# Optimization experiments

Hardware: AMD Instinct MI355X
Metric: run time of the kernel (lower is better)

The kernel has to match this reference:

```python
import jax, jax.numpy as jnp
import numpy as np

INPUT, HIDDEN = 15, 20

def setup_inputs() -> dict:
    key = jax.random.key(0)
    k1, k2, k3, k4, k5 = jax.random.split(key, 5)
    B, T = 4096, 512
    s = 1.0 / np.sqrt(HIDDEN)  # torch default uniform init bound
    feature = jax.random.normal(k1, (B, T, INPUT), dtype=jnp.float32)
    W_ih = jax.random.uniform(k2, (HIDDEN, INPUT), jnp.float32, -s, s)
    W_hh = jax.random.uniform(k3, (HIDDEN, HIDDEN), jnp.float32, -s, s)
    b_ih = jax.random.uniform(k4, (HIDDEN,), jnp.float32, -s, s)
    b_hh = jax.random.uniform(k5, (HIDDEN,), jnp.float32, -s, s)
    return {"feature": feature, "W_ih": W_ih, "W_hh": W_hh, "b_ih": b_ih, "b_hh": b_hh}

def reference(feature, W_ih, W_hh, b_ih, b_hh):
    # h_t = tanh(x_t @ W_ih^T + b_ih + h_{t-1} @ W_hh^T + b_hh)
    B, T, _ = feature.shape
    # precompute input projections for all timesteps: [T, B, H]
    xp = jnp.einsum('bti,hi->tbh', feature, W_ih) + (b_ih + b_hh)
    h0 = jnp.zeros((B, HIDDEN), dtype=feature.dtype)
    def step(h, x_t):
        h_new = jnp.tanh(x_t + h @ W_hh.T)
        return h_new, None
    hn, _ = jax.lax.scan(step, h0, xp)
    return hn  # [B, H] == hn.squeeze() for num_layers=1
```

## Files before the change

kernel.cpp:

```cpp
#include <hip/hip_runtime.h>
#include <cstddef>


typedef float g4 __attribute__((ext_vector_type(4), aligned(4)));
typedef float g2 __attribute__((ext_vector_type(2), aligned(4)));
typedef _Float16 h2  __attribute__((ext_vector_type(2)));
typedef _Float16 v8h __attribute__((ext_vector_type(8)));
typedef _Float16 v4h __attribute__((ext_vector_type(4)));

#define TT 512
#define IN 15
#define HD 20
#define CH 32
#define NCH (TT / CH)
#define XROW 16
#define XGRP (CH * XROW + 16)
#define XBUF (3 * XGRP)
#define HROW 24

#define P2(v, i) __builtin_shufflevector(v, v, 2 * (i), 2 * (i) + 1)
#define FD(acc, p, w) acc = __builtin_amdgcn_fdot2(p, w, acc, false)

__global__ __launch_bounds__(64) void rnn_fused(
    const float* __restrict__ feature, const float* __restrict__ W_ih,
    const float* __restrict__ W_hh, const float* __restrict__ b_ih,
    const float* __restrict__ b_hh, float* __restrict__ out, int B) {
  __shared__ __align__(16) _Float16 xh[2 * XBUF];
  __shared__ __align__(16) _Float16 hh[4 * HROW];

  const int lane = threadIdx.x;
  const int g = lane / HD;
  const int j = lane - g * HD;
  const int gx = (g < 3) ? g : 2;
  const int bid = blockIdx.x;
  const int b = bid * 3 + g;

  if (lane < 48) ((float*)hh)[lane] = 0.f;

  h2 wih[8];
  {
    const float* wr = W_ih + j * IN;
#pragma unroll
    for (int i = 0; i < 7; ++i)
      wih[i] = (h2){(_Float16)wr[2 * i], (_Float16)wr[2 * i + 1]};
    wih[7] = (h2){(_Float16)wr[14], (_Float16)0.f};
  }
  h2 whh[10];
  {
    const float* wr = W_hh + j * HD;
#pragma unroll
    for (int i = 0; i < 10; ++i)
      whh[i] = (h2){(_Float16)wr[2 * i], (_Float16)wr[2 * i + 1]};
  }
  const float bias = b_ih[j] + b_hh[j];

  const int grA = lane >> 5;
  const int tcA = lane & 31;
  const int bc = B - 1;
  const int bA = min(bid * 3 + grA, bc);
  const int bB = min(bid * 3 + 2, bc);
  const float* baseA = feature + ((size_t)bA * TT + tcA) * IN;
  const float* baseB = feature + ((size_t)bB * TT + tcA) * IN;

  g4 rA0, rA1, rA2; g2 rA3; float rA4;
  g4 rB0, rB1, rB2; g2 rB3; float rB4;

  auto issue = [&](int t0) {
    const float* s = baseA + (size_t)t0 * IN;
    rA0 = *(const g4*)(s);      rA1 = *(const g4*)(s + 4);
    rA2 = *(const g4*)(s + 8);  rA3 = *(const g2*)(s + 12);
    rA4 = s[14];
    if (lane < 32) {
      const float* s2 = baseB + (size_t)t0 * IN;
      rB0 = *(const g4*)(s2);     rB1 = *(const g4*)(s2 + 4);
      rB2 = *(const g4*)(s2 + 8); rB3 = *(const g2*)(s2 + 12);
      rB4 = s2[14];
    }
  };
  auto commit = [&](int bsel) {
    v8h lo = {(_Float16)rA0.x, (_Float16)rA0.y, (_Float16)rA0.z, (_Float16)rA0.w,
              (_Float16)rA1.x, (_Float16)rA1.y, (_Float16)rA1.z, (_Float16)rA1.w};
    v8h hi = {(_Float16)rA2.x, (_Float16)rA2.y, (_Float16)rA2.z, (_Float16)rA2.w,
              (_Float16)rA3.x, (_Float16)rA3.y, (_Float16)rA4,   (_Float16)0.f};
    _Float16* d = xh + bsel * XBUF + grA * XGRP + tcA * XROW;
    *(v8h*)d = lo; *((v8h*)d + 1) = hi;
    if (lane < 32) {
      v8h lo2 = {(_Float16)rB0.x, (_Float16)rB0.y, (_Float16)rB0.z, (_Float16)rB0.w,
                 (_Float16)rB1.x, (_Float16)rB1.y, (_Float16)rB1.z, (_Float16)rB1.w};
      v8h hi2 = {(_Float16)rB2.x, (_Float16)rB2.y, (_Float16)rB2.z, (_Float16)rB2.w,
                 (_Float16)rB3.x, (_Float16)rB3.y, (_Float16)rB4,   (_Float16)0.f};
      _Float16* d2 = xh + bsel * XBUF + 2 * XGRP + tcA * XROW;
      *(v8h*)d2 = lo2; *((v8h*)d2 + 1) = hi2;
    }
  };

  issue(0);
  commit(0);

  float hn = 0.f;
  const _Float16* hrd = hh + g * HROW;
  _Float16* hwr = hh + g * HROW + j;
  for (int c = 0; c < NCH; ++c) {
    if (c + 1 < NCH) issue((c + 1) * CH);
    const _Float16* xg = xh + (c & 1) * XBUF + gx * XGRP;
#pragma unroll 4
    for (int tc = 0; tc < CH; ++tc) {
      v8h ha = *(const v8h*)hrd;
      v8h hb = *(const v8h*)(hrd + 8);
      v4h hc = *(const v4h*)(hrd + 16);
      const v8h* xp = (const v8h*)(xg + tc * XROW);
      v8h xa = xp[0], xb = xp[1];
      float a0 = bias, a1 = 0.f, a2 = 0.f, a3 = 0.f;
      FD(a0, P2(xa, 0), wih[0]); FD(a1, P2(xa, 1), wih[1]);
      FD(a2, P2(xa, 2), wih[2]); FD(a3, P2(xa, 3), wih[3]);
      FD(a0, P2(xb, 0), wih[4]); FD(a1, P2(xb, 1), wih[5]);
      FD(a2, P2(xb, 2), wih[6]); FD(a3, P2(xb, 3), wih[7]);
      FD(a0, P2(ha, 0), whh[0]); FD(a1, P2(ha, 1), whh[1]);
      FD(a2, P2(ha, 2), whh[2]); FD(a3, P2(ha, 3), whh[3]);
      FD(a0, P2(hb, 0), whh[4]); FD(a1, P2(hb, 1), whh[5]);
      FD(a2, P2(hb, 2), whh[6]); FD(a3, P2(hb, 3), whh[7]);
      FD(a0, P2(hc, 0), whh[8]); FD(a1, P2(hc, 1), whh[9]);
      float s = (a0 + a1) + (a2 + a3);
      float e = exp2f(s * 2.8853900817779268f);
      hn = 1.f - 2.f * __builtin_amdgcn_rcpf(1.f + e);
      *hwr = (_Float16)hn;
    }
    if (c + 1 < NCH) commit((c + 1) & 1);
  }
  if (g < 3 && b < B) out[(size_t)b * HD + j] = hn;
}

extern "C" void kernel_launch(void* const* d_in, const int* in_sizes, int n_in,
                              void* d_out, int out_size, void* d_ws, size_t ws_size,
                              hipStream_t stream) {
  const float* feature = (const float*)d_in[0];
  const float* W_ih    = (const float*)d_in[1];
  const float* W_hh    = (const float*)d_in[2];
  const float* b_ih    = (const float*)d_in[3];
  const float* b_hh    = (const float*)d_in[4];
  float* out = (float*)d_out;
  const int B = in_sizes[0] / (TT * IN);
  const int grid = (B + 2) / 3;
  rnn_fused<<<grid, 64, 0, stream>>>(feature, W_ih, W_hh, b_ih, b_hh, out, B);
}
```

Before: 232.3 us.

## Rewrite RNN recurrence with MFMA over 16-batch tiles per wavefront

Replaces the per-lane fdot2 recurrence, which ran three batches per 64-lane block, with MFMA matrix instructions. Each wavefront now handles 16 batches, and the hidden state stays in registers as the MFMA B operand, so there is no LDS round trip for h. The input projection for the next step is computed with a separate MFMA while the current step runs, and the tanh scale is folded into the weights. Input staging is reworked into 16-step double-buffered chunks. The grid shrinks to B/16 blocks, so there are far fewer waves to fill the GPU, and every step now depends on MFMA latency.

```diff
diff --git a/kernel.cpp b/kernel.cpp
--- a/kernel.cpp
+++ b/kernel.cpp
@@ -2,132 +2,151 @@
 #include <cstddef>
 
 
+typedef float f4 __attribute__((ext_vector_type(4)));
 typedef float g4 __attribute__((ext_vector_type(4), aligned(4)));
-typedef float g2 __attribute__((ext_vector_type(2), aligned(4)));
-typedef _Float16 h2  __attribute__((ext_vector_type(2)));
+typedef _Float16 h2 __attribute__((ext_vector_type(2)));
+typedef _Float16 v4h __attribute__((ext_vector_type(4)));
 typedef _Float16 v8h __attribute__((ext_vector_type(8)));
-typedef _Float16 v4h __attribute__((ext_vector_type(4)));
+typedef __fp16 p2 __attribute__((ext_vector_type(2)));
 
 #define TT 512
 #define IN 15
 #define HD 20
-#define CH 32
-#define NCH (TT / CH)
-#define XROW 16
-#define XGRP (CH * XROW + 16)
-#define XBUF (3 * XGRP)
-#define HROW 24
+#define NB 16
+#define CT 16
+#define NC (TT / CT)
+#define XCHUNK (CT * 256)
 
-#define P2(v, i) __builtin_shufflevector(v, v, 2 * (i), 2 * (i) + 1)
-#define FD(acc, p, w) acc = __builtin_amdgcn_fdot2(p, w, acc, false)
+__device__ __forceinline__ h2 pk2(float a, float b) {
+  p2 r = __builtin_amdgcn_cvt_pkrtz(a, b);
+  return __builtin_bit_cast(h2, r);
+}
+__device__ __forceinline__ v4h cat4(h2 a, h2 b) {
+  return __builtin_shufflevector(a, b, 0, 1, 2, 3);
+}
+__device__ __forceinline__ v8h cat8(v4h a, v4h b) {
+  return __builtin_shufflevector(a, b, 0, 1, 2, 3, 4, 5, 6, 7);
+}
 
-__global__ __launch_bounds__(64) void rnn_fused(
+__global__ __launch_bounds__(64) void rnn_mfma(
     const float* __restrict__ feature, const float* __restrict__ W_ih,
     const float* __restrict__ W_hh, const float* __restrict__ b_ih,
     const float* __restrict__ b_hh, float* __restrict__ out, int B) {
-  __shared__ __align__(16) _Float16 xh[2 * XBUF];
-  __shared__ __align__(16) _Float16 hh[4 * HROW];
+  __shared__ __align__(16) _Float16 xh[2 * XCHUNK];
 
-  const int lane = threadIdx.x;
-  const int g = lane / HD;
-  const int j = lane - g * HD;
-  const int gx = (g < 3) ? g : 2;
-  const int bid = blockIdx.x;
-  const int b = bid * 3 + g;
+  const int l = threadIdx.x;
+  const int G = l >> 4;
+  const int mf = l & 15;
+  const int b0 = blockIdx.x * NB;
 
-  if (lane < 48) ((float*)hh)[lane] = 0.f;
+  const float K2 = 2.8853900817779268f;
 
-  h2 wih[8];
-  {
-    const float* wr = W_ih + j * IN;
+  const int jPa = 8 * (mf >> 2) + (mf & 3);
+  const int jQa = jPa + 4;
+
+  v8h AhhP, AhhQ;
 #pragma unroll
-    for (int i = 0; i < 7; ++i)
-      wih[i] = (h2){(_Float16)wr[2 * i], (_Float16)wr[2 * i + 1]};
-    wih[7] = (h2){(_Float16)wr[14], (_Float16)0.f};
+  for (int i = 0; i < 8; ++i) {
+    const int k = 8 * G + i;
+    AhhP[i] = (_Float16)((jPa < HD && k < HD) ? K2 * W_hh[jPa * HD + k] : 0.f);
+    AhhQ[i] = (_Float16)((jQa < HD && k < HD) ? K2 * W_hh[jQa * HD + k] : 0.f);
   }
-  h2 whh[10];
-  {
-    const float* wr = W_hh + j * HD;
+  v4h AihP, AihQ;
 #pragma unroll
-    for (int i = 0; i < 10; ++i)
-      whh[i] = (h2){(_Float16)wr[2 * i], (_Float16)wr[2 * i + 1]};
+  for (int i = 0; i < 4; ++i) {
+    const int k = 4 * G + i;
+    AihP[i] = (_Float16)((jPa < HD && k < IN) ? K2 * W_ih[jPa * IN + k] : 0.f);
+    AihQ[i] = (_Float16)((jQa < HD && k < IN) ? K2 * W_ih[jQa * IN + k] : 0.f);
   }
-  const float bias = b_ih[j] + b_hh[j];
+  f4 biasP, biasQ;
+#pragma unroll
+  for (int r = 0; r < 4; ++r) {
+    const int jp = 8 * G + r, jq = jp + 4;
+    biasP[r] = (jp < HD) ? K2 * (b_ih[jp] + b_hh[jp]) : 0.f;
+    biasQ[r] = (jq < HD) ? K2 * (b_ih[jq] + b_hh[jq]) : 0.f;
+  }
 
-  const int grA = lane >> 5;
-  const int tcA = lane & 31;
-  const int bc = B - 1;
-  const int bA = min(bid * 3 + grA, bc);
-  const int bB = min(bid * 3 + 2, bc);
-  const float* baseA = feature + ((size_t)bA * TT + tcA) * IN;
-  const float* baseB = feature + ((size_t)bB * TT + tcA) * IN;
+  const int sc = l >> 2;
+  const int st = l & 3;
+  const float* srow = feature + (size_t)min(b0 + sc, B - 1) * TT * IN;
+  g4 R0[4], R1[4], R2[4], R3[4];
 
-  g4 rA0, rA1, rA2; g2 rA3; float rA4;
-  g4 rB0, rB1, rB2; g2 rB3; float rB4;
-
-  auto issue = [&](int t0) {
-    const float* s = baseA + (size_t)t0 * IN;
-    rA0 = *(const g4*)(s);      rA1 = *(const g4*)(s + 4);
-    rA2 = *(const g4*)(s + 8);  rA3 = *(const g2*)(s + 12);
-    rA4 = s[14];
-    if (lane < 32) {
-      const float* s2 = baseB + (size_t)t0 * IN;
-      rB0 = *(const g4*)(s2);     rB1 = *(const g4*)(s2 + 4);
-      rB2 = *(const g4*)(s2 + 8); rB3 = *(const g2*)(s2 + 12);
-      rB4 = s2[14];
+  auto issue = [&](int ch) {
+    const int t0 = ch * CT;
+#pragma unroll
+    for (int q = 0; q < 4; ++q) {
+      const float* s = srow + (size_t)(t0 + st + 4 * q) * IN;
+      R0[q] = *(const g4*)s;
+      R1[q] = *(const g4*)(s + 4);
+      R2[q] = *(const g4*)(s + 8);
+      R3[q] = *(const g4*)(s + 11);
     }
   };
-  auto commit = [&](int bsel) {
-    v8h lo = {(_Float16)rA0.x, (_Float16)rA0.y, (_Float16)rA0.z, (_Float16)rA0.w,
-              (_Float16)rA1.x, (_Float16)rA1.y, (_Float16)rA1.z, (_Float16)rA1.w};
-    v8h hi = {(_Float16)rA2.x, (_Float16)rA2.y, (_Float16)rA2.z, (_Float16)rA2.w,
-              (_Float16)rA3.x, (_Float16)rA3.y, (_Float16)rA4,   (_Float16)0.f};
-    _Float16* d = xh + bsel * XBUF + grA * XGRP + tcA * XROW;
-    *(v8h*)d = lo; *((v8h*)d + 1) = hi;
-    if (lane < 32) {
-      v8h lo2 = {(_Float16)rB0.x, (_Float16)rB0.y, (_Float16)rB0.z, (_Float16)rB0.w,
-                 (_Float16)rB1.x, (_Float16)rB1.y, (_Float16)rB1.z, (_Float16)rB1.w};
-      v8h hi2 = {(_Float16)rB2.x, (_Float16)rB2.y, (_Float16)rB2.z, (_Float16)rB2.w,
-                 (_Float16)rB3.x, (_Float16)rB3.y, (_Float16)rB4,   (_Float16)0.f};
-      _Float16* d2 = xh + bsel * XBUF + 2 * XGRP + tcA * XROW;
-      *(v8h*)d2 = lo2; *((v8h*)d2 + 1) = hi2;
+  auto commit = [&](int ch) {
+    _Float16* base = xh + (ch & 1) * XCHUNK + sc * 4;
+#pragma unroll
+    for (int q = 0; q < 4; ++q) {
+      _Float16* row = base + (st + 4 * q) * 256;
+      *(v4h*)(row)       = cat4(pk2(R0[q].x, R0[q].y), pk2(R0[q].z, R0[q].w));
+      *(v4h*)(row + 64)  = cat4(pk2(R1[q].x, R1[q].y), pk2(R1[q].z, R1[q].w));
+      *(v4h*)(row + 128) = cat4(pk2(R2[q].x, R2[q].y), pk2(R2[q].z, R2[q].w));
+      *(v4h*)(row + 192) = cat4(pk2(R3[q].y, R3[q].z), pk2(R3[q].w, 0.f));
     }
   };
 
   issue(0);
   commit(0);
 
-  float hn = 0.f;
-  const _Float16* hrd = hh + g * HROW;
-  _Float16* hwr = hh + g * HROW + j;
-  for (int c = 0; c < NCH; ++c) {
-    if (c + 1 < NCH) issue((c + 1) * CH);
-    const _Float16* xg = xh + (c & 1) * XBUF + gx * XGRP;
-#pragma unroll 4
-    for (int tc = 0; tc < CH; ++tc) {
-      v8h ha = *(const v8h*)hrd;
-      v8h hb = *(const v8h*)(hrd + 8);
-      v4h hc = *(const v4h*)(hrd + 16);
-      const v8h* xp = (const v8h*)(xg + tc * XROW);
-      v8h xa = xp[0], xb = xp[1];
-      float a0 = bias, a1 = 0.f, a2 = 0.f, a3 = 0.f;
-      FD(a0, P2(xa, 0), wih[0]); FD(a1, P2(xa, 1), wih[1]);
-      FD(a2, P2(xa, 2), wih[2]); FD(a3, P2(xa, 3), wih[3]);
-      FD(a0, P2(xb, 0), wih[4]); FD(a1, P2(xb, 1), wih[5]);
-      FD(a2, P2(xb, 2), wih[6]); FD(a3, P2(xb, 3), wih[7]);
-      FD(a0, P2(ha, 0), whh[0]); FD(a1, P2(ha, 1), whh[1]);
-      FD(a2, P2(ha, 2), whh[2]); FD(a3, P2(ha, 3), whh[3]);
-      FD(a0, P2(hb, 0), whh[4]); FD(a1, P2(hb, 1), whh[5]);
-      FD(a2, P2(hb, 2), whh[6]); FD(a3, P2(hb, 3), whh[7]);
-      FD(a0, P2(hc, 0), whh[8]); FD(a1, P2(hc, 1), whh[9]);
-      float s = (a0 + a1) + (a2 + a3);
-      float e = exp2f(s * 2.8853900817779268f);
-      hn = 1.f - 2.f * __builtin_amdgcn_rcpf(1.f + e);
-      *hwr = (_Float16)hn;
+  v4h Xc = *(const v4h*)(xh + l * 4);
+  f4 cxPc = __builtin_amdgcn_mfma_f32_16x16x16f16(AihP, Xc, biasP, 0, 0, 0);
+  f4 cxQc = __builtin_amdgcn_mfma_f32_16x16x16f16(AihQ, Xc, biasQ, 0, 0, 0);
+  Xc = *(const v4h*)(xh + 256 + l * 4);
+  int xoff = 2 * 256 + l * 4;
+
+  v8h Bh;
+#pragma unroll
+  for (int i = 0; i < 8; ++i) Bh[i] = (_Float16)0.f;
+
+  float tPk[4], tQk[4];
+
+  for (int ch = 0; ch < NC; ++ch) {
+    if (ch + 1 < NC) issue(ch + 1);
+#pragma unroll
+    for (int tc = 0; tc < CT; ++tc) {
+      if (tc == 8 && ch + 1 < NC) {
+        commit(ch + 1);
+        asm volatile("" ::: "memory");
+      }
+      f4 aP = __builtin_amdgcn_mfma_f32_16x16x32_f16(AhhP, Bh, cxPc, 0, 0, 0);
+      f4 aQ = __builtin_amdgcn_mfma_f32_16x16x32_f16(AhhQ, Bh, cxQc, 0, 0, 0);
+      v4h Xn = *(const v4h*)(xh + xoff);
+      xoff = (xoff + 256) & (2 * XCHUNK - 1);
+      cxPc = __builtin_amdgcn_mfma_f32_16x16x16f16(AihP, Xc, biasP, 0, 0, 0);
+      cxQc = __builtin_amdgcn_mfma_f32_16x16x16f16(AihQ, Xc, biasQ, 0, 0, 0);
+      Xc = Xn;
+#pragma unroll
+      for (int r = 0; r < 4; ++r) {
+        const float eP = exp2f(aP[r]);
+        tPk[r] = 1.f - 2.f * __builtin_amdgcn_rcpf(1.f + eP);
+        const float eQ = exp2f(aQ[r]);
+        tQk[r] = 1.f - 2.f * __builtin_amdgcn_rcpf(1.f + eQ);
+      }
+      Bh = cat8(cat4(pk2(tPk[0], tPk[1]), pk2(tPk[2], tPk[3])),
+                cat4(pk2(tQk[0], tQk[1]), pk2(tQk[2], tQk[3])));
     }
-    if (c + 1 < NCH) commit((c + 1) & 1);
   }
-  if (g < 3 && b < B) out[(size_t)b * HD + j] = hn;
+
+  const int batch = b0 + mf;
+  if (batch < B) {
+    float* orow = out + (size_t)batch * HD;
+#pragma unroll
+    for (int r = 0; r < 4; ++r) {
+      const int jp = 8 * G + r;
+      if (jp < HD) orow[jp] = tPk[r];
+      const int jq = jp + 4;
+      if (jq < HD) orow[jq] = tQk[r];
+    }
+  }
 }
 
 extern "C" void kernel_launch(void* const* d_in, const int* in_sizes, int n_in,
@@ -140,6 +159,6 @@
   const float* b_hh    = (const float*)d_in[4];
   float* out = (float*)d_out;
   const int B = in_sizes[0] / (TT * IN);
-  const int grid = (B + 2) / 3;
-  rnn_fused<<<grid, 64, 0, stream>>>(feature, W_ih, W_hh, b_ih, b_hh, out, B);
+  const int grid = (B + NB - 1) / NB;
+  rnn_mfma<<<grid, 64, 0, stream>>>(feature, W_ih, W_hh, b_ih, b_hh, out, B);
 }
```

New measurement: 288.5 us. +24.2%, slower.
